# Performance work log

Measured on AMD Instinct MI355X. Metric: run time of the kernel, lower is better.

The kernel has to match this reference:

```python
import jax, jax.numpy as jnp
import numpy as np

NUM_CLASSES = 3
STRIDES = (8, 16, 32)


def _decode(out, stride):
    # out: [B, 5+C, H, W] -> [B, H*W, 5+C] decoded to image coords; also return grid [H*W, 2]
    B, C, H, W = out.shape
    yv, xv = jnp.meshgrid(jnp.arange(H), jnp.arange(W), indexing='ij')
    grid = jnp.stack([xv, yv], -1).reshape(H * W, 2).astype(out.dtype)
    o = out.reshape(B, C, H * W).transpose(0, 2, 1)
    xy = (o[..., :2] + grid[None]) * stride
    wh = jnp.exp(o[..., 2:4]) * stride
    return jnp.concatenate([xy, wh, o[..., 4:]], -1), grid


def _pairwise_iou(gt, pr):
    # gt [G,4], pr [A,4], cxcywh -> iou [G,A]
    tl = jnp.maximum(gt[:, None, :2] - gt[:, None, 2:] / 2, pr[None, :, :2] - pr[None, :, 2:] / 2)
    br = jnp.minimum(gt[:, None, :2] + gt[:, None, 2:] / 2, pr[None, :, :2] + pr[None, :, 2:] / 2)
    en = (tl < br).all(-1).astype(gt.dtype)
    area_i = jnp.prod(br - tl, -1) * en
    area_u = jnp.prod(gt[:, None, 2:], -1) + jnp.prod(pr[None, :, 2:], -1) - area_i
    return area_i / (area_u + 1e-16)


def _iou_loss(pred, target):
    # elementwise IOUloss (loss_type='iou'): 1 - iou^2, shapes [..., 4]
    tl = jnp.maximum(pred[..., :2] - pred[..., 2:] / 2, target[..., :2] - target[..., 2:] / 2)
    br = jnp.minimum(pred[..., :2] + pred[..., 2:] / 2, target[..., :2] + target[..., 2:] / 2)
    en = (tl < br).all(-1).astype(pred.dtype)
    area_i = jnp.prod(br - tl, -1) * en
    area_u = jnp.prod(pred[..., 2:], -1) + jnp.prod(target[..., 2:], -1) - area_i
    iou = area_i / (area_u + 1e-16)
    return 1.0 - iou ** 2


def _bce_logits(x, y):
    # stable BCEWithLogits, reduction='none'
    return jnp.maximum(x, 0) - x * y + jnp.log1p(jnp.exp(-jnp.abs(x)))


def _assign(gt_boxes, gt_cls, box_p, cls_p, obj_p, xs, ys, strides):
    # SimOTA for one image. gt_boxes [G,4], gt_cls [G], box_p [A,4], cls_p [A,C], obj_p [A,1]
    G = gt_boxes.shape[0]
    C = cls_p.shape[-1]
    xc = (xs + 0.5) * strides  # [A] anchor centers in image coords
    yc = (ys + 0.5) * strides
    # anchors inside gt boxes
    gl = gt_boxes[:, 0:1] - gt_boxes[:, 2:3] / 2
    gr = gt_boxes[:, 0:1] + gt_boxes[:, 2:3] / 2
    gt_ = gt_boxes[:, 1:2] - gt_boxes[:, 3:4] / 2
    gb = gt_boxes[:, 1:2] + gt_boxes[:, 3:4] / 2
    in_box = (xc[None] > gl) & (xc[None] < gr) & (yc[None] > gt_) & (yc[None] < gb)  # [G,A]
    # anchors inside center radius 2.5 * stride
    r = 2.5
    in_ctr = ((xc[None] > gt_boxes[:, 0:1] - r * strides[None]) &
              (xc[None] < gt_boxes[:, 0:1] + r * strides[None]) &
              (yc[None] > gt_boxes[:, 1:2] - r * strides[None]) &
              (yc[None] < gt_boxes[:, 1:2] + r * strides[None]))
    cand = in_box.any(0) | in_ctr.any(0)  # [A] candidate anchors (fg_mask)
    in_both = in_box & in_ctr  # [G,A]
    ious = jnp.where(cand[None], _pairwise_iou(gt_boxes, box_p), 0.0)
    iou_cost = -jnp.log(ious + 1e-8)
    p = jnp.sqrt(jax.nn.sigmoid(cls_p) * jax.nn.sigmoid(obj_p))  # [A,C]
    y = jax.nn.one_hot(gt_cls, C, dtype=p.dtype)  # [G,C]
    cls_cost = -(jnp.einsum('gc,ac->ga', y, jnp.log(p + 1e-8)) +
                 jnp.einsum('gc,ac->ga', 1 - y, jnp.log(1 - p + 1e-8)))
    cost = cls_cost + 3.0 * iou_cost + 1e5 * (~in_both).astype(p.dtype)
    cost = jnp.where(cand[None], cost, 1e9)
    # dynamic-k: k_g = clamp(int(sum of top-10 ious), 1)
    topk_ious, _ = jax.lax.top_k(ious, 10)
    dyn_k = jnp.clip(topk_ious.sum(-1).astype(jnp.int32), 1, None)  # [G]
    ranks = jnp.argsort(jnp.argsort(cost, axis=1), axis=1)
    matching = (ranks < dyn_k[:, None]) & cand[None]  # [G,A]
    # resolve anchors matched to multiple gts by min cost
    multi = matching.sum(0) > 1  # [A]
    best = jnp.arange(G)[:, None] == jnp.argmin(cost, axis=0)[None]  # [G,A]
    matching = jnp.where(multi[None], best, matching)
    fg = matching.any(0)  # [A]
    matched_gt = jnp.argmax(matching, axis=0)  # [A]
    pred_iou = (matching.astype(p.dtype) * ious).sum(0)  # [A]
    cls_t = jax.nn.one_hot(gt_cls[matched_gt], C, dtype=p.dtype) * pred_iou[:, None]  # [A,C]
    reg_t = gt_boxes[matched_gt]  # [A,4]
    return fg, cls_t, reg_t


def _forward(p3, p4, p5, mask_inputs, labels, input_images, mask_labels, now_epoch):
    outs, grids, str_list = [], [], []
    for o, s in zip((p3, p4, p5), STRIDES):
        dec, g = _decode(o, float(s))
        outs.append(dec)
        grids.append(g)
        str_list.append(jnp.full((g.shape[0],), float(s), dtype=dec.dtype))
    outputs = jnp.concatenate(outs, 1)  # [B, A, 5+C]
    xs = jnp.concatenate([g[:, 0] for g in grids], 0)  # [A]
    ys = jnp.concatenate([g[:, 1] for g in grids], 0)
    strides = jnp.concatenate(str_list, 0)
    box_p = outputs[..., :4]
    obj_p = outputs[..., 4:5]
    cls_p = outputs[..., 5:]
    gt_boxes = labels[..., :4]
    gt_cls = labels[..., 4].astype(jnp.int32)
    fg, cls_t, reg_t = jax.vmap(_assign, in_axes=(0, 0, 0, 0, 0, None, None, None))(
        gt_boxes, gt_cls, box_p, cls_p, obj_p, xs, ys, strides)
    # assignment is @torch.no_grad() in the original
    fg, cls_t, reg_t = jax.lax.stop_gradient((fg, cls_t, reg_t))
    fgf = fg.astype(outputs.dtype)  # [B,A]
    num_fg = jnp.maximum(fgf.sum(), 1.0)
    loss_iou = (_iou_loss(box_p, reg_t) * fgf).sum()
    loss_obj = _bce_logits(obj_p[..., 0], fgf).sum()
    loss_cls = (_bce_logits(cls_p, cls_t) * fgf[..., None]).sum()
    # segmentation losses: CE (mean NLL over pixels) + Dice
    logp = jax.nn.log_softmax(mask_inputs, axis=1)  # [B,C,H,W]
    ce = -jnp.take_along_axis(logp, mask_labels[:, None].astype(jnp.int32), axis=1).mean()
    sm = jax.nn.softmax(mask_inputs, axis=1).transpose(0, 2, 3, 1)  # [B,H,W,C]
    oh = jax.nn.one_hot(mask_labels, NUM_CLASSES + 1, dtype=sm.dtype)[..., :NUM_CLASSES]
    tp = (oh * sm).sum((0, 1, 2))
    fp = sm.sum((0, 1, 2)) - tp
    fn = oh.sum((0, 1, 2)) - tp
    smooth = 1e-5
    dice = 1.0 - jnp.mean((2 * tp + smooth) / (2 * tp + fn + fp + smooth))  # beta=1
    loss_mask = ce + dice
    loss_sc = jnp.zeros((), outputs.dtype)  # is_sc=False
    reg_w = 5.0
    total = (reg_w * loss_iou + loss_obj + loss_cls + loss_sc) / num_fg + loss_mask
    return jnp.stack([total, reg_w * loss_iou / num_fg, loss_obj / num_fg,
                      loss_cls / num_fg, loss_mask, loss_sc / num_fg])


def setup_inputs() -> dict:
    key = jax.random.key(0)
    ks = jax.random.split(key, 8)
    B, IMG, G = 8, 1024, 20
    C5 = NUM_CLASSES + 5
    p3 = jax.random.normal(ks[0], (B, C5, 128, 128), jnp.float32)
    p4 = jax.random.normal(ks[1], (B, C5, 64, 64), jnp.float32)
    p5 = jax.random.normal(ks[2], (B, C5, 32, 32), jnp.float32)
    mask_inputs = jax.random.normal(ks[3], (B, NUM_CLASSES, IMG, IMG), jnp.float32)
    cxy = jax.random.uniform(ks[4], (B, G, 2), jnp.float32, 64.0, float(IMG - 64))
    wh = jax.random.uniform(ks[5], (B, G, 2), jnp.float32, 16.0, 256.0)
    cls = jax.random.randint(ks[6], (B, G, 1), 0, NUM_CLASSES).astype(jnp.float32)
    labels = jnp.concatenate([cxy, wh, cls], -1)  # [B,G,5] (cx,cy,w,h,class)
    input_images = jax.random.uniform(ks[7], (B, 1, IMG, IMG), jnp.float32)
    mask_labels = jax.random.randint(jax.random.fold_in(key, 9), (B, IMG, IMG), 0, NUM_CLASSES)
    return {"p3": p3, "p4": p4, "p5": p5, "mask_inputs": mask_inputs,
            "labels": labels, "input_images": input_images,
            "mask_labels": mask_labels, "now_epoch": 0}


def reference(p3, p4, p5, mask_inputs, labels, input_images, mask_labels, now_epoch):
    return _forward(p3, p4, p5, mask_inputs, labels, input_images, mask_labels, now_epoch)
```

## Files before the change

### kernel.cpp

```cpp
#include <hip/hip_runtime.h>
#include <cfloat>

constexpr int A_TOT = 21504;
constexpr int NB    = 8;
constexpr int NG    = 20;
constexpr int HW_M  = 1 << 20;
constexpr int SPLIT = 16;
constexpr int CHUNK = A_TOT / SPLIT;
constexpr int MBLK  = 2048;
constexpr int MSLC  = MBLK / 4;

constexpr float L2E = 1.44269504088896340736f;
constexpr float LN2 = 0.69314718055994530942f;

constexpr size_t OFF_DEC  = 0;
constexpr size_t SZ_DEC   = (size_t)NB * A_TOT * 8;
constexpr size_t OFF_IOUS = OFF_DEC + SZ_DEC;
constexpr size_t SZ_GA    = (size_t)NB * NG * A_TOT;
constexpr size_t OFF_COST = OFF_IOUS + SZ_GA;
constexpr size_t OFF_THRC = OFF_COST + SZ_GA;
constexpr size_t OFF_THRI = OFF_THRC + NB * NG;
constexpr size_t OFF_CAND = OFF_THRI + NB * NG;
constexpr size_t OFF_PM   = OFF_CAND + (NB * A_TOT) / 4;
constexpr size_t OFF_PK   = OFF_PM + 672 * 4;
constexpr size_t OFF_PV   = OFF_PK + (size_t)MBLK * 10;
constexpr size_t SZ_PART  = (size_t)NB * NG * SPLIT * 10;
constexpr size_t OFF_PC   = OFF_PV + SZ_PART;
constexpr size_t OFF_PI   = OFF_PC + SZ_PART;

__device__ __forceinline__ float hw_exp2(float x) { return __builtin_amdgcn_exp2f(x); }
__device__ __forceinline__ float hw_log2(float x) { return __builtin_amdgcn_logf(x); }
__device__ __forceinline__ float fexp(float x) { return hw_exp2(x * L2E); }
__device__ __forceinline__ float flog(float x) { return hw_log2(x) * LN2; }
__device__ __forceinline__ float frcp(float x) { return __builtin_amdgcn_rcpf(x); }
__device__ __forceinline__ float fsig(float x) { return frcp(1.f + fexp(-x)); }
__device__ __forceinline__ float fbce(float x, float y) {
  float t = hw_exp2(-fabsf(x) * L2E);
  return fmaxf(x, 0.f) - x * y + LN2 * hw_log2(1.f + t);
}
__device__ __forceinline__ void anchor_geom(int a, int& hw, int& lw, float& st) {
  if (a < 16384)      { hw = a;         lw = 7; st = 8.f;  }
  else if (a < 20480) { hw = a - 16384; lw = 6; st = 16.f; }
  else                { hw = a - 20480; lw = 5; st = 32.f; }
}

__device__ __forceinline__ void merge_desc(float* a, const float* b) {
  float m[16];
  m[0] = a[0]; m[1] = a[1]; m[2] = a[2]; m[3] = a[3]; m[4] = a[4]; m[5] = a[5];
  m[6] = fmaxf(a[6], b[9]); m[7] = fmaxf(a[7], b[8]);
  m[8] = fmaxf(a[8], b[7]); m[9] = fmaxf(a[9], b[6]);
  m[10] = b[5]; m[11] = b[4]; m[12] = b[3]; m[13] = b[2]; m[14] = b[1]; m[15] = b[0];
#pragma unroll
  for (int s = 8; s >= 1; s >>= 1) {
#pragma unroll
    for (int i = 0; i < 16; ++i) {
      if (!(i & s)) {
        float hi = fmaxf(m[i], m[i + s]);
        float lo = fminf(m[i], m[i + s]);
        m[i] = hi; m[i + s] = lo;
      }
    }
  }
#pragma unroll
  for (int j = 0; j < 10; ++j) a[j] = m[j];
}

__device__ __forceinline__ void merge_asc(float* ac, int* ai,
                                          const float* bc, const int* bi) {
  float mc[16]; int mi[16];
#pragma unroll
  for (int i = 0; i < 6; ++i) { mc[i] = ac[i]; mi[i] = ai[i]; }
#pragma unroll
  for (int i = 6; i < 10; ++i) {
    float c2 = bc[15 - i]; int i2 = bi[15 - i];
    bool ta = (ac[i] < c2) || (ac[i] == c2 && ai[i] < i2);
    mc[i] = ta ? ac[i] : c2; mi[i] = ta ? ai[i] : i2;
  }
  mc[10] = bc[5]; mi[10] = bi[5]; mc[11] = bc[4]; mi[11] = bi[4];
  mc[12] = bc[3]; mi[12] = bi[3]; mc[13] = bc[2]; mi[13] = bi[2];
  mc[14] = bc[1]; mi[14] = bi[1]; mc[15] = bc[0]; mi[15] = bi[0];
#pragma unroll
  for (int s = 8; s >= 1; s >>= 1) {
#pragma unroll
    for (int i = 0; i < 16; ++i) {
      if (!(i & s)) {
        float cA = mc[i], cB = mc[i + s];
        int   iA = mi[i], iB = mi[i + s];
        bool ta = (cB < cA) || (cB == cA && iB < iA);
        mc[i]     = ta ? cB : cA; mi[i]     = ta ? iB : iA;
        mc[i + s] = ta ? cA : cB; mi[i + s] = ta ? iA : iB;
      }
    }
  }
#pragma unroll
  for (int j = 0; j < 10; ++j) { ac[j] = mc[j]; ai[j] = mi[j]; }
}

__device__ __forceinline__ void mask_block(int vblk,
    const float* __restrict__ mi, const int* __restrict__ ml,
    float* __restrict__ pk, int tid) {
  int b  = vblk >> 8;
  int g0 = (vblk & 255) << 10;
  const float* base0 = mi + (size_t)b * 3 * HW_M + (size_t)g0 * 4;
  const int*   lbase = ml + ((size_t)b << 20) + (size_t)g0 * 4;

  float4 x0[4], x1[4], x2[4]; int4 lb[4];
#pragma unroll
  for (int u = 0; u < 4; ++u) {
    size_t off = (size_t)(tid + u * 256) * 4;
    x0[u] = *(const float4*)(base0 + off);
    x1[u] = *(const float4*)(base0 + HW_M + off);
    x2[u] = *(const float4*)(base0 + 2 * HW_M + off);
    lb[u] = *(const int4*)(lbase + off);
  }

  float ce = 0.f, tp0 = 0, tp1 = 0, tp2 = 0;
  float ss0 = 0, ss1 = 0, c0 = 0, c1 = 0;

  auto proc = [&](float v0, float v1, float v2, int l) {
    float e0 = hw_exp2(v0 * L2E);
    float e1 = hw_exp2(v1 * L2E);
    float e2 = hw_exp2(v2 * L2E);
    float sum = e0 + e1 + e2;
    float inv = __builtin_amdgcn_rcpf(sum);
    float lse = hw_log2(sum) * LN2;
    float s0 = e0 * inv, s1 = e1 * inv;
    ss0 += s0; ss1 += s1;
    bool l0 = (l == 0), l1 = (l == 1);
    float vl = l0 ? v0 : (l1 ? v1 : v2);
    float el = l0 ? e0 : (l1 ? e1 : e2);
    float sl = el * inv;
    ce += vl - lse;
    tp0 += l0 ? sl : 0.f;
    tp1 += l1 ? sl : 0.f;
    tp2 += (!l0 && !l1) ? sl : 0.f;
    c0 += l0 ? 1.f : 0.f;
    c1 += l1 ? 1.f : 0.f;
  };

#pragma unroll
  for (int u = 0; u < 4; ++u) {
    proc(x0[u].x, x1[u].x, x2[u].x, lb[u].x);
    proc(x0[u].y, x1[u].y, x2[u].y, lb[u].y);
    proc(x0[u].z, x1[u].z, x2[u].z, lb[u].z);
    proc(x0[u].w, x1[u].w, x2[u].w, lb[u].w);
  }
  float ss2 = 16.f - ss0 - ss1;
  float c2 = 16.f - c0 - c1;

  __shared__ float scr[4][10];
  float vals[10] = { ce, tp0, tp1, tp2, ss0, ss1, ss2, c0, c1, c2 };
#pragma unroll
  for (int k = 0; k < 10; ++k) {
    float v = vals[k];
#pragma unroll
    for (int off = 32; off > 0; off >>= 1) v += __shfl_down(v, off, 64);
    if ((tid & 63) == 0) scr[tid >> 6][k] = v;
  }
  __syncthreads();
  if (tid == 0) {
#pragma unroll
    for (int k = 0; k < 10; ++k)
      pk[(size_t)vblk * 10 + k] = scr[0][k] + scr[1][k] + scr[2][k] + scr[3][k];
  }
}

__global__ __launch_bounds__(256) void k_cost_mask(
    const float* __restrict__ p3, const float* __restrict__ p4,
    const float* __restrict__ p5, const float* __restrict__ labels,
    float* __restrict__ dec, float* __restrict__ ious,
    float* __restrict__ cost, unsigned char* __restrict__ cand,
    const float* __restrict__ mi, const int* __restrict__ ml,
    float* __restrict__ pk) {
  int bi = blockIdx.x, tid = threadIdx.x;
  if (bi >= 672) { mask_block(bi - 672, mi, ml, pk, tid); return; }
  int b = bi / 84, cx = bi - b * 84;

  __shared__ float gt[NG][5];
  if (tid < NG * 5) ((float*)gt)[tid] = labels[b * NG * 5 + tid];
  __syncthreads();
  int a = cx * 256 + tid;

  int hw, lw; float st;
  anchor_geom(a, hw, lw, st);
  const float* src; int HW;
  if (a < 16384)      { src = p3; HW = 16384; }
  else if (a < 20480) { src = p4; HW = 4096;  }
  else                { src = p5; HW = 1024;  }
  int x = hw & ((1 << lw) - 1), y = hw >> lw;
  const float* c0 = src + (size_t)b * 8 * HW + hw;
  float o0 = c0[0];
  float o1 = c0[(size_t)HW];
  float o2 = c0[(size_t)2 * HW];
  float o3 = c0[(size_t)3 * HW];
  float o4 = c0[(size_t)4 * HW];
  float o5 = c0[(size_t)5 * HW];
  float o6 = c0[(size_t)6 * HW];
  float o7 = c0[(size_t)7 * HW];
  float px = (o0 + (float)x) * st, py = (o1 + (float)y) * st;
  float pw = fexp(o2) * st,        ph = fexp(o3) * st;
  {
    float4* dst = (float4*)(dec + ((size_t)b * A_TOT + a) * 8);
    dst[0] = make_float4(px, py, pw, ph);
    dst[1] = make_float4(o4, o5, o6, o7);
  }

  float xc = ((float)x + 0.5f) * st, yc = ((float)y + 0.5f) * st;

  float so = fsig(o4);
  float cc0, cc1, cc2, S;
  {
    float q0 = sqrtf(fsig(o5) * so);
    float q1 = sqrtf(fsig(o6) * so);
    float q2 = sqrtf(fsig(o7) * so);
    float lg0 = flog(q0 + 1e-8f), lg1 = flog(q1 + 1e-8f), lg2 = flog(q2 + 1e-8f);
    float m0 = flog(1.f - q0 + 1e-8f), m1 = flog(1.f - q1 + 1e-8f), m2 = flog(1.f - q2 + 1e-8f);
    S = m0 + m1 + m2;
    cc0 = lg0 - m0; cc1 = lg1 - m1; cc2 = lg2 - m2;
  }

  float iouv[NG];
  unsigned bothMask = 0;
  bool anyBox = false, anyCtr = false;
  float hpw = pw * 0.5f, hph = ph * 0.5f;
  float plx = px - hpw, prx = px + hpw, pty = py - hph, pby = py + hph;
  float parea = pw * ph;
  float r = 2.5f * st;

#pragma unroll
  for (int g = 0; g < NG; ++g) {
    float gx = gt[g][0], gy = gt[g][1], gw = gt[g][2], gh = gt[g][3];
    float hgw = gw * 0.5f, hgh = gh * 0.5f;
    float glx = gx - hgw, grx = gx + hgw, gty = gy - hgh, gby = gy + hgh;
    bool ib = (xc > glx) && (xc < grx) && (yc > gty) && (yc < gby);
    bool ic = (xc > gx - r) && (xc < gx + r) && (yc > gy - r) && (yc < gy + r);
    anyBox |= ib; anyCtr |= ic;
    if (ib && ic) bothMask |= (1u << g);
    float tlx = fmaxf(glx, plx), brx = fminf(grx, prx);
    float tly = fmaxf(gty, pty), bry = fminf(gby, pby);
    float en = ((tlx < brx) && (tly < bry)) ? 1.f : 0.f;
    float ai = (brx - tlx) * (bry - tly) * en;
    float au = gw * gh + parea - ai;
    iouv[g] = ai / (au + 1e-16f);
  }
  bool cd = anyBox || anyCtr;
  cand[(size_t)b * A_TOT + a] = cd ? 1 : 0;

#pragma unroll
  for (int g = 0; g < NG; ++g) {
    float iv = cd ? iouv[g] : 0.f;
    int cg = (int)gt[g][4];
    float ccg = (cg == 0) ? cc0 : ((cg == 1) ? cc1 : cc2);
    float c = -(ccg + S) - 3.f * flog(iv + 1e-8f) +
              (((bothMask >> g) & 1u) ? 0.f : 100000.f);
    size_t idx = ((size_t)(b * NG + g)) * A_TOT + a;
    ious[idx] = iv;
    cost[idx] = cd ? c : 1e9f;
  }
}

__global__ __launch_bounds__(256) void k_topk_mask(
    const float* __restrict__ ious, const float* __restrict__ cost,
    float* __restrict__ pV, float* __restrict__ pC, int* __restrict__ pI,
    const float* __restrict__ mi, const int* __restrict__ ml,
    float* __restrict__ pk) {
  int bi = blockIdx.x, tid = threadIdx.x;
  if (bi >= 640) { mask_block(MSLC + (bi - 640), mi, ml, pk, tid); return; }

  int w = tid >> 6, lane = tid & 63;
  int t = bi * 4 + w;
  int b = t / (NG * SPLIT);
  int rem = t - b * (NG * SPLIT);
  int g = rem / SPLIT;
  int s = rem - g * SPLIT;
  int row = b * NG + g;
  int lo = s * CHUNK;
  const float4* iou4 = (const float4*)(ious + (size_t)row * A_TOT + lo);
  const float4* cst4 = (const float4*)(cost + (size_t)row * A_TOT + lo);
  constexpr int NG4 = CHUNK / 4;

  float tv[10];
  float tc[10]; int ti[10];
#pragma unroll
  for (int j = 0; j < 10; ++j) { tv[j] = -1e30f; tc[j] = FLT_MAX; ti[j] = 0x7fffffff; }

  auto insV = [&](float v) {
    if (v > tv[9]) {
#pragma unroll
      for (int j = 0; j < 10; ++j)
        if (v > tv[j]) { float t2 = tv[j]; tv[j] = v; v = t2; }
    }
  };
  auto insC = [&](float c, int ii) {
    if ((c < tc[9]) || (c == tc[9] && ii < ti[9])) {
#pragma unroll
      for (int j = 0; j < 10; ++j) {
        bool lt = (c < tc[j]) || (c == tc[j] && ii < ti[j]);
        if (lt) {
          float t2 = tc[j]; tc[j] = c; c = t2;
          int t3 = ti[j]; ti[j] = ii; ii = t3;
        }
      }
    }
  };

#pragma unroll 1
  for (int grp = lane; grp < NG4; grp += 64) {
    float4 v4 = iou4[grp];
    float4 c4 = cst4[grp];
    int base = lo + grp * 4;
    insV(v4.x); insV(v4.y); insV(v4.z); insV(v4.w);
    insC(c4.x, base); insC(c4.y, base + 1); insC(c4.z, base + 2); insC(c4.w, base + 3);
  }

#pragma unroll 1
  for (int d = 1; d < 64; d <<= 1) {
    float bv[10];
#pragma unroll
    for (int j = 0; j < 10; ++j) bv[j] = __shfl_xor(tv[j], d, 64);
    merge_desc(tv, bv);
  }
#pragma unroll 1
  for (int d = 1; d < 64; d <<= 1) {
    float bc[10]; int bi2[10];
#pragma unroll
    for (int j = 0; j < 10; ++j) {
      bc[j] = __shfl_xor(tc[j], d, 64);
      bi2[j] = __shfl_xor(ti[j], d, 64);
    }
    merge_asc(tc, ti, bc, bi2);
  }

  if (lane == 0) {
    size_t base = ((size_t)row * SPLIT + s) * 10;
#pragma unroll
    for (int j = 0; j < 10; ++j) {
      pV[base + j] = tv[j];
      pC[base + j] = tc[j];
      pI[base + j] = ti[j];
    }
  }
}

__global__ __launch_bounds__(256) void k_merge_mask(
    const float* __restrict__ pV, const float* __restrict__ pC,
    const int* __restrict__ pI, float* __restrict__ thrC, int* __restrict__ thrI,
    const float* __restrict__ mi, const int* __restrict__ ml,
    float* __restrict__ pk) {
  int bi = blockIdx.x, tid = threadIdx.x;
  if (bi >= 160) { mask_block(2 * MSLC + (bi - 160), mi, ml, pk, tid); return; }
  int row = bi;
  constexpr int NC = SPLIT * 10;
  __shared__ float sV[NC], sC[NC];
  __shared__ int   sI[NC];
  __shared__ float slot[10];
  __shared__ int kS;

  if (tid < NC) {
    size_t base = (size_t)row * NC + tid;
    sV[tid] = pV[base];
    sC[tid] = pC[base];
    sI[tid] = pI[base];
  }
  __syncthreads();

  float myV = 0.f, myC = 0.f; int myI = 0, rankV = 0;
  if (tid < NC) {
    myV = sV[tid]; myC = sC[tid]; myI = sI[tid];
    for (int j = 0; j < NC; ++j) {
      float v = sV[j];
      rankV += ((v > myV) || (v == myV && j < tid)) ? 1 : 0;
    }
  }
  if (tid < NC && rankV < 10) slot[rankV] = myV;
  __syncthreads();
  if (tid == 0) {
    float sum = 0.f;
#pragma unroll
    for (int j = 0; j < 10; ++j) sum += slot[j];
    int k = (int)sum; if (k < 1) k = 1;
    kS = k;
  }
  __syncthreads();
  if (tid < NC) {
    int rankC = 0;
    for (int j = 0; j < NC; ++j) {
      float c = sC[j];
      rankC += ((c < myC) || (c == myC && sI[j] < myI)) ? 1 : 0;
    }
    if (rankC == kS - 1) { thrC[row] = myC; thrI[row] = myI; }
  }
}

__global__ __launch_bounds__(256) void k_match_mask(
    const float* __restrict__ dec, const float* __restrict__ labels,
    const float* __restrict__ ious, const float* __restrict__ cost,
    const unsigned char* __restrict__ cand,
    const float* __restrict__ thrC, const int* __restrict__ thrI,
    float* __restrict__ pm,
    const float* __restrict__ mi, const int* __restrict__ ml,
    float* __restrict__ pk) {
  int bi = blockIdx.x, tid = threadIdx.x;
  if (bi >= 672) { mask_block(3 * MSLC + (bi - 672), mi, ml, pk, tid); return; }
  int b = bi / 84, cx = bi - b * 84;

  __shared__ float gt[NG][5];
  __shared__ float tC[NG];
  __shared__ int   tI[NG];
  if (tid < NG * 5) ((float*)gt)[tid] = labels[b * NG * 5 + tid];
  if (tid >= 128 && tid < 128 + NG) tC[tid - 128] = thrC[b * NG + tid - 128];
  if (tid >= 160 && tid < 160 + NG) tI[tid - 160] = thrI[b * NG + tid - 160];
  __syncthreads();
  int a = cx * 256 + tid;

  bool cd = cand[(size_t)b * A_TOT + a] != 0;
  int cnt = 0, firstg = -1, gmin = 0;
  float minc = FLT_MAX, pisum = 0.f, iou_gmin = 0.f;
#pragma unroll
  for (int g = 0; g < NG; ++g) {
    size_t idx = ((size_t)(b * NG + g)) * A_TOT + a;
    float c = cost[idx];
    float iv = ious[idx];
    if (c < minc) { minc = c; gmin = g; iou_gmin = iv; }
    bool m = cd && ((c < tC[g]) || (c == tC[g] && a <= tI[g]));
    if (m) { cnt++; if (firstg < 0) firstg = g; pisum += iv; }
  }
  if (cnt > 1) { firstg = gmin; pisum = iou_gmin; }
  bool fg = cnt > 0;

  const float4* dp = (const float4*)(dec + ((size_t)b * A_TOT + a) * 8);
  float4 d0 = dp[0], d1 = dp[1];
  float l_obj = fbce(d1.x, fg ? 1.f : 0.f);
  float l_iou = 0.f, l_cls = 0.f, nfg = fg ? 1.f : 0.f;
  if (fg) {
    float gx = gt[firstg][0], gy = gt[firstg][1];
    float gw = gt[firstg][2], gh = gt[firstg][3];
    int cg = (int)gt[firstg][4];
    float px = d0.x, py = d0.y, pw = d0.z, ph = d0.w;
    float tlx = fmaxf(px - pw * 0.5f, gx - gw * 0.5f);
    float brx = fminf(px + pw * 0.5f, gx + gw * 0.5f);
    float tly = fmaxf(py - ph * 0.5f, gy - gh * 0.5f);
    float bry = fminf(py + ph * 0.5f, gy + gh * 0.5f);
    float en = ((tlx < brx) && (tly < bry)) ? 1.f : 0.f;
    float ai = (brx - tlx) * (bry - tly) * en;
    float au = pw * ph + gw * gh - ai;
    float iou = ai / (au + 1e-16f);
    l_iou = 1.f - iou * iou;
    l_cls  = fbce(d1.y, (cg == 0) ? pisum : 0.f);
    l_cls += fbce(d1.z, (cg == 1) ? pisum : 0.f);
    l_cls += fbce(d1.w, (cg == 2) ? pisum : 0.f);
  }

  __shared__ float scr2[4][4];
  float vals[4] = { nfg, l_iou, l_obj, l_cls };
#pragma unroll
  for (int k = 0; k < 4; ++k) {
    float v = vals[k];
#pragma unroll
    for (int off = 32; off > 0; off >>= 1) v += __shfl_down(v, off, 64);
    if ((tid & 63) == 0) scr2[tid >> 6][k] = v;
  }
  __syncthreads();
  if (tid == 0) {
#pragma unroll
    for (int k = 0; k < 4; ++k)
      pm[(size_t)bi * 4 + k] = scr2[0][k] + scr2[1][k] + scr2[2][k] + scr2[3][k];
  }
}

__device__ __forceinline__ float bsum256(float v, float* scr) {
#pragma unroll
  for (int off = 32; off > 0; off >>= 1) v += __shfl_down(v, off, 64);
  __syncthreads();
  if ((threadIdx.x & 63) == 0) scr[threadIdx.x >> 6] = v;
  __syncthreads();
  return scr[0] + scr[1] + scr[2] + scr[3];
}

__global__ __launch_bounds__(256) void k_final(
    const float* __restrict__ pm, const float* __restrict__ pk,
    float* __restrict__ out) {
  __shared__ float scr[4];
  int tid = threadIdx.x;
  float t0 = 0, t1 = 0, t2 = 0, t3 = 0;
  for (int r = tid; r < 672; r += 256) {
    t0 += pm[(size_t)r * 4 + 0];
    t1 += pm[(size_t)r * 4 + 1];
    t2 += pm[(size_t)r * 4 + 2];
    t3 += pm[(size_t)r * 4 + 3];
  }
  float u[10] = {0,0,0,0,0,0,0,0,0,0};
  for (int r = tid; r < MBLK; r += 256) {
#pragma unroll
    for (int k = 0; k < 10; ++k) u[k] += pk[(size_t)r * 10 + k];
  }
  float S_nfg = bsum256(t0, scr);
  float S_iou = bsum256(t1, scr);
  float S_obj = bsum256(t2, scr);
  float S_cls = bsum256(t3, scr);
  float S_ce  = bsum256(u[0], scr);
  float S_tp0 = bsum256(u[1], scr);
  float S_tp1 = bsum256(u[2], scr);
  float S_tp2 = bsum256(u[3], scr);
  float S_ss0 = bsum256(u[4], scr);
  float S_ss1 = bsum256(u[5], scr);
  float S_ss2 = bsum256(u[6], scr);
  float S_c0  = bsum256(u[7], scr);
  float S_c1  = bsum256(u[8], scr);
  float S_c2  = bsum256(u[9], scr);

  if (tid == 0) {
    float nfg = fmaxf(S_nfg, 1.f);
    float o1 = 5.f * S_iou / nfg;
    float o2 = S_obj / nfg;
    float o3 = S_cls / nfg;
    float ce = -S_ce / (float)((long long)NB << 20);
    float tps[3] = { S_tp0, S_tp1, S_tp2 };
    float sss[3] = { S_ss0, S_ss1, S_ss2 };
    float cns[3] = { S_c0, S_c1, S_c2 };
    float ds = 0.f;
#pragma unroll
    for (int c = 0; c < 3; ++c) {
      float tp = tps[c];
      float fp = sss[c] - tp;
      float fn = cns[c] - tp;
      ds += (2.f * tp + 1e-5f) / (2.f * tp + fn + fp + 1e-5f);
    }
    float dice = 1.f - ds / 3.f;
    float o4 = ce + dice;
    out[0] = o1 + o2 + o3 + o4;
    out[1] = o1;
    out[2] = o2;
    out[3] = o3;
    out[4] = o4;
    out[5] = 0.f;
  }
}

extern "C" void kernel_launch(void* const* d_in, const int* in_sizes, int n_in,
                              void* d_out, int out_size, void* d_ws, size_t ws_size,
                              hipStream_t stream) {
  const float* p3     = (const float*)d_in[0];
  const float* p4     = (const float*)d_in[1];
  const float* p5     = (const float*)d_in[2];
  const float* mi     = (const float*)d_in[3];
  const float* labels = (const float*)d_in[4];
  const int*   ml     = (const int*)d_in[6];

  float* ws   = (float*)d_ws;
  float* dec  = ws + OFF_DEC;
  float* ious = ws + OFF_IOUS;
  float* cost = ws + OFF_COST;
  float* thrC = ws + OFF_THRC;
  int*   thrI = (int*)(ws + OFF_THRI);
  unsigned char* cand = (unsigned char*)(ws + OFF_CAND);
  float* pm   = ws + OFF_PM;
  float* pk   = ws + OFF_PK;
  float* pV   = ws + OFF_PV;
  float* pC   = ws + OFF_PC;
  int*   pI   = (int*)(ws + OFF_PI);
  float* out  = (float*)d_out;

  k_cost_mask <<<672 + MSLC, 256, 0, stream>>>(p3, p4, p5, labels, dec, ious,
                                               cost, cand, mi, ml, pk);
  k_topk_mask <<<640 + MSLC, 256, 0, stream>>>(ious, cost, pV, pC, pI,
                                               mi, ml, pk);
  k_merge_mask<<<160 + MSLC, 256, 0, stream>>>(pV, pC, pI, thrC, thrI,
                                               mi, ml, pk);
  k_match_mask<<<672 + MSLC, 256, 0, stream>>>(dec, labels, ious, cost, cand,
                                               thrC, thrI, pm, mi, ml, pk);
  k_final<<<1, 256, 0, stream>>>(pm, pk, out);
}
```

Before: 91.40 us.

## Fuse top-k split and merge into one kernel, recompute decode in match

Merges the per-chunk top-k and the merge kernels into a single kernel in which one block per (image, gt) row scans the whole anchor row and merges the four wave results in shared memory. This removes a launch and the partial-result round trip. The match kernel now reloads the raw predictions and recomputes the decode, candidate mask and IoUs instead of reading the dec, cand and ious buffers, so those workspace writes and reads are dropped. The mask-loss block split across the three kernels is rebalanced to 680/688/680. The cost is that 160 blocks now each do a long serial scan, and the match kernel repeats the IoU computation.

Result: slower. 123.1 us (+34.7%).

```diff
diff --git a/kernel.cpp b/kernel.cpp
--- a/kernel.cpp
+++ b/kernel.cpp
@@ -5,28 +5,22 @@
 constexpr int NB    = 8;
 constexpr int NG    = 20;
 constexpr int HW_M  = 1 << 20;
-constexpr int SPLIT = 16;
-constexpr int CHUNK = A_TOT / SPLIT;
+constexpr int NGRP4 = A_TOT / 4;
 constexpr int MBLK  = 2048;
-constexpr int MSLC  = MBLK / 4;
+constexpr int MS1   = 680;
+constexpr int MS2   = 688;
+constexpr int MS3   = 680;
 
 constexpr float L2E = 1.44269504088896340736f;
 constexpr float LN2 = 0.69314718055994530942f;
 
-constexpr size_t OFF_DEC  = 0;
-constexpr size_t SZ_DEC   = (size_t)NB * A_TOT * 8;
-constexpr size_t OFF_IOUS = OFF_DEC + SZ_DEC;
 constexpr size_t SZ_GA    = (size_t)NB * NG * A_TOT;
+constexpr size_t OFF_IOUS = 0;
 constexpr size_t OFF_COST = OFF_IOUS + SZ_GA;
 constexpr size_t OFF_THRC = OFF_COST + SZ_GA;
 constexpr size_t OFF_THRI = OFF_THRC + NB * NG;
-constexpr size_t OFF_CAND = OFF_THRI + NB * NG;
-constexpr size_t OFF_PM   = OFF_CAND + (NB * A_TOT) / 4;
+constexpr size_t OFF_PM   = OFF_THRI + NB * NG;
 constexpr size_t OFF_PK   = OFF_PM + 672 * 4;
-constexpr size_t OFF_PV   = OFF_PK + (size_t)MBLK * 10;
-constexpr size_t SZ_PART  = (size_t)NB * NG * SPLIT * 10;
-constexpr size_t OFF_PC   = OFF_PV + SZ_PART;
-constexpr size_t OFF_PI   = OFF_PC + SZ_PART;
 
 __device__ __forceinline__ float hw_exp2(float x) { return __builtin_amdgcn_exp2f(x); }
 __device__ __forceinline__ float hw_log2(float x) { return __builtin_amdgcn_logf(x); }
@@ -95,6 +89,7 @@
 #pragma unroll
   for (int j = 0; j < 10; ++j) { ac[j] = mc[j]; ai[j] = mi[j]; }
 }
+
 
 __device__ __forceinline__ void mask_block(int vblk,
     const float* __restrict__ mi, const int* __restrict__ ml,
@@ -168,8 +163,7 @@
 __global__ __launch_bounds__(256) void k_cost_mask(
     const float* __restrict__ p3, const float* __restrict__ p4,
     const float* __restrict__ p5, const float* __restrict__ labels,
-    float* __restrict__ dec, float* __restrict__ ious,
-    float* __restrict__ cost, unsigned char* __restrict__ cand,
+    float* __restrict__ ious, float* __restrict__ cost,
     const float* __restrict__ mi, const int* __restrict__ ml,
     float* __restrict__ pk) {
   int bi = blockIdx.x, tid = threadIdx.x;
@@ -199,11 +193,6 @@
   float o7 = c0[(size_t)7 * HW];
   float px = (o0 + (float)x) * st, py = (o1 + (float)y) * st;
   float pw = fexp(o2) * st,        ph = fexp(o3) * st;
-  {
-    float4* dst = (float4*)(dec + ((size_t)b * A_TOT + a) * 8);
-    dst[0] = make_float4(px, py, pw, ph);
-    dst[1] = make_float4(o4, o5, o6, o7);
-  }
 
   float xc = ((float)x + 0.5f) * st, yc = ((float)y + 0.5f) * st;
 
@@ -244,7 +233,6 @@
     iouv[g] = ai / (au + 1e-16f);
   }
   bool cd = anyBox || anyCtr;
-  cand[(size_t)b * A_TOT + a] = cd ? 1 : 0;
 
 #pragma unroll
   for (int g = 0; g < NG; ++g) {
@@ -259,25 +247,16 @@
   }
 }
 
-__global__ __launch_bounds__(256) void k_topk_mask(
+__global__ __launch_bounds__(256) void k_topkmerge_mask(
     const float* __restrict__ ious, const float* __restrict__ cost,
-    float* __restrict__ pV, float* __restrict__ pC, int* __restrict__ pI,
+    float* __restrict__ thrC, int* __restrict__ thrI,
     const float* __restrict__ mi, const int* __restrict__ ml,
     float* __restrict__ pk) {
   int bi = blockIdx.x, tid = threadIdx.x;
-  if (bi >= 640) { mask_block(MSLC + (bi - 640), mi, ml, pk, tid); return; }
-
-  int w = tid >> 6, lane = tid & 63;
-  int t = bi * 4 + w;
-  int b = t / (NG * SPLIT);
-  int rem = t - b * (NG * SPLIT);
-  int g = rem / SPLIT;
-  int s = rem - g * SPLIT;
-  int row = b * NG + g;
-  int lo = s * CHUNK;
-  const float4* iou4 = (const float4*)(ious + (size_t)row * A_TOT + lo);
-  const float4* cst4 = (const float4*)(cost + (size_t)row * A_TOT + lo);
-  constexpr int NG4 = CHUNK / 4;
+  if (bi >= 160) { mask_block(MS1 + (bi - 160), mi, ml, pk, tid); return; }
+  int row = bi;
+  const float4* iou4 = (const float4*)(ious + (size_t)row * A_TOT);
+  const float4* cst4 = (const float4*)(cost + (size_t)row * A_TOT);
 
   float tv[10];
   float tc[10]; int ti[10];
@@ -305,10 +284,10 @@
   };
 
 #pragma unroll 1
-  for (int grp = lane; grp < NG4; grp += 64) {
+  for (int grp = tid; grp < NGRP4; grp += 256) {
     float4 v4 = iou4[grp];
     float4 c4 = cst4[grp];
-    int base = lo + grp * 4;
+    int base = grp * 4;
     insV(v4.x); insV(v4.y); insV(v4.z); insV(v4.w);
     insC(c4.x, base); insC(c4.y, base + 1); insC(c4.z, base + 2); insC(c4.w, base + 3);
   }
@@ -331,48 +310,29 @@
     merge_asc(tc, ti, bc, bi2);
   }
 
-  if (lane == 0) {
-    size_t base = ((size_t)row * SPLIT + s) * 10;
-#pragma unroll
-    for (int j = 0; j < 10; ++j) {
-      pV[base + j] = tv[j];
-      pC[base + j] = tc[j];
-      pI[base + j] = ti[j];
-    }
-  }
-}
-
-__global__ __launch_bounds__(256) void k_merge_mask(
-    const float* __restrict__ pV, const float* __restrict__ pC,
-    const int* __restrict__ pI, float* __restrict__ thrC, int* __restrict__ thrI,
-    const float* __restrict__ mi, const int* __restrict__ ml,
-    float* __restrict__ pk) {
-  int bi = blockIdx.x, tid = threadIdx.x;
-  if (bi >= 160) { mask_block(2 * MSLC + (bi - 160), mi, ml, pk, tid); return; }
-  int row = bi;
-  constexpr int NC = SPLIT * 10;
-  __shared__ float sV[NC], sC[NC];
-  __shared__ int   sI[NC];
+  __shared__ float sV[40], sC[40];
+  __shared__ int   sI[40];
   __shared__ float slot[10];
   __shared__ int kS;
-
-  if (tid < NC) {
-    size_t base = (size_t)row * NC + tid;
-    sV[tid] = pV[base];
-    sC[tid] = pC[base];
-    sI[tid] = pI[base];
-  }
-  __syncthreads();
-
-  float myV = 0.f, myC = 0.f; int myI = 0, rankV = 0;
-  if (tid < NC) {
-    myV = sV[tid]; myC = sC[tid]; myI = sI[tid];
-    for (int j = 0; j < NC; ++j) {
+  int w = tid >> 6;
+  if ((tid & 63) == 0) {
+#pragma unroll
+    for (int j = 0; j < 10; ++j) {
+      sV[w * 10 + j] = tv[j];
+      sC[w * 10 + j] = tc[j];
+      sI[w * 10 + j] = ti[j];
+    }
+  }
+  __syncthreads();
+  if (tid < 40) {
+    float myV = sV[tid];
+    int rankV = 0;
+    for (int j = 0; j < 40; ++j) {
       float v = sV[j];
       rankV += ((v > myV) || (v == myV && j < tid)) ? 1 : 0;
     }
-  }
-  if (tid < NC && rankV < 10) slot[rankV] = myV;
+    if (rankV < 10) slot[rankV] = myV;
+  }
   __syncthreads();
   if (tid == 0) {
     float sum = 0.f;
@@ -382,9 +342,10 @@
     kS = k;
   }
   __syncthreads();
-  if (tid < NC) {
+  if (tid < 40) {
+    float myC = sC[tid]; int myI = sI[tid];
     int rankC = 0;
-    for (int j = 0; j < NC; ++j) {
+    for (int j = 0; j < 40; ++j) {
       float c = sC[j];
       rankC += ((c < myC) || (c == myC && sI[j] < myI)) ? 1 : 0;
     }
@@ -393,15 +354,15 @@
 }
 
 __global__ __launch_bounds__(256) void k_match_mask(
-    const float* __restrict__ dec, const float* __restrict__ labels,
-    const float* __restrict__ ious, const float* __restrict__ cost,
-    const unsigned char* __restrict__ cand,
+    const float* __restrict__ p3, const float* __restrict__ p4,
+    const float* __restrict__ p5, const float* __restrict__ labels,
+    const float* __restrict__ cost,
     const float* __restrict__ thrC, const int* __restrict__ thrI,
     float* __restrict__ pm,
     const float* __restrict__ mi, const int* __restrict__ ml,
     float* __restrict__ pk) {
   int bi = blockIdx.x, tid = threadIdx.x;
-  if (bi >= 672) { mask_block(3 * MSLC + (bi - 672), mi, ml, pk, tid); return; }
+  if (bi >= 672) { mask_block(MS1 + MS2 + (bi - 672), mi, ml, pk, tid); return; }
   int b = bi / 84, cx = bi - b * 84;
 
   __shared__ float gt[NG][5];
@@ -413,14 +374,57 @@
   __syncthreads();
   int a = cx * 256 + tid;
 
-  bool cd = cand[(size_t)b * A_TOT + a] != 0;
+  int hw, lw; float st;
+  anchor_geom(a, hw, lw, st);
+  const float* src; int HW;
+  if (a < 16384)      { src = p3; HW = 16384; }
+  else if (a < 20480) { src = p4; HW = 4096;  }
+  else                { src = p5; HW = 1024;  }
+  int x = hw & ((1 << lw) - 1), y = hw >> lw;
+  const float* c0p = src + (size_t)b * 8 * HW + hw;
+  float o0 = c0p[0];
+  float o1 = c0p[(size_t)HW];
+  float o2 = c0p[(size_t)2 * HW];
+  float o3 = c0p[(size_t)3 * HW];
+  float o4 = c0p[(size_t)4 * HW];
+  float o5 = c0p[(size_t)5 * HW];
+  float o6 = c0p[(size_t)6 * HW];
+  float o7 = c0p[(size_t)7 * HW];
+  float px = (o0 + (float)x) * st, py = (o1 + (float)y) * st;
+  float pw = fexp(o2) * st,        ph = fexp(o3) * st;
+
+  float xc = ((float)x + 0.5f) * st, yc = ((float)y + 0.5f) * st;
+
+  float iouv[NG];
+  bool anyBox = false, anyCtr = false;
+  float hpw = pw * 0.5f, hph = ph * 0.5f;
+  float plx = px - hpw, prx = px + hpw, pty = py - hph, pby = py + hph;
+  float parea = pw * ph;
+  float r = 2.5f * st;
+#pragma unroll
+  for (int g = 0; g < NG; ++g) {
+    float gx = gt[g][0], gy = gt[g][1], gw = gt[g][2], gh = gt[g][3];
+    float hgw = gw * 0.5f, hgh = gh * 0.5f;
+    float glx = gx - hgw, grx = gx + hgw, gty = gy - hgh, gby = gy + hgh;
+    bool ib = (xc > glx) && (xc < grx) && (yc > gty) && (yc < gby);
+    bool ic = (xc > gx - r) && (xc < gx + r) && (yc > gy - r) && (yc < gy + r);
+    anyBox |= ib; anyCtr |= ic;
+    float tlx = fmaxf(glx, plx), brx = fminf(grx, prx);
+    float tly = fmaxf(gty, pty), bry = fminf(gby, pby);
+    float en = ((tlx < brx) && (tly < bry)) ? 1.f : 0.f;
+    float ai = (brx - tlx) * (bry - tly) * en;
+    float au = gw * gh + parea - ai;
+    iouv[g] = ai / (au + 1e-16f);
+  }
+  bool cd = anyBox || anyCtr;
+
   int cnt = 0, firstg = -1, gmin = 0;
   float minc = FLT_MAX, pisum = 0.f, iou_gmin = 0.f;
 #pragma unroll
   for (int g = 0; g < NG; ++g) {
     size_t idx = ((size_t)(b * NG + g)) * A_TOT + a;
     float c = cost[idx];
-    float iv = ious[idx];
+    float iv = cd ? iouv[g] : 0.f;
     if (c < minc) { minc = c; gmin = g; iou_gmin = iv; }
     bool m = cd && ((c < tC[g]) || (c == tC[g] && a <= tI[g]));
     if (m) { cnt++; if (firstg < 0) firstg = g; pisum += iv; }
@@ -428,15 +432,12 @@
   if (cnt > 1) { firstg = gmin; pisum = iou_gmin; }
   bool fg = cnt > 0;
 
-  const float4* dp = (const float4*)(dec + ((size_t)b * A_TOT + a) * 8);
-  float4 d0 = dp[0], d1 = dp[1];
-  float l_obj = fbce(d1.x, fg ? 1.f : 0.f);
+  float l_obj = fbce(o4, fg ? 1.f : 0.f);
   float l_iou = 0.f, l_cls = 0.f, nfg = fg ? 1.f : 0.f;
   if (fg) {
     float gx = gt[firstg][0], gy = gt[firstg][1];
     float gw = gt[firstg][2], gh = gt[firstg][3];
     int cg = (int)gt[firstg][4];
-    float px = d0.x, py = d0.y, pw = d0.z, ph = d0.w;
     float tlx = fmaxf(px - pw * 0.5f, gx - gw * 0.5f);
     float brx = fminf(px + pw * 0.5f, gx + gw * 0.5f);
     float tly = fmaxf(py - ph * 0.5f, gy - gh * 0.5f);
@@ -446,9 +447,9 @@
     float au = pw * ph + gw * gh - ai;
     float iou = ai / (au + 1e-16f);
     l_iou = 1.f - iou * iou;
-    l_cls  = fbce(d1.y, (cg == 0) ? pisum : 0.f);
-    l_cls += fbce(d1.z, (cg == 1) ? pisum : 0.f);
-    l_cls += fbce(d1.w, (cg == 2) ? pisum : 0.f);
+    l_cls  = fbce(o5, (cg == 0) ? pisum : 0.f);
+    l_cls += fbce(o6, (cg == 1) ? pisum : 0.f);
+    l_cls += fbce(o7, (cg == 2) ? pisum : 0.f);
   }
 
   __shared__ float scr2[4][4];
@@ -548,26 +549,19 @@
   const int*   ml     = (const int*)d_in[6];
 
   float* ws   = (float*)d_ws;
-  float* dec  = ws + OFF_DEC;
   float* ious = ws + OFF_IOUS;
   float* cost = ws + OFF_COST;
   float* thrC = ws + OFF_THRC;
   int*   thrI = (int*)(ws + OFF_THRI);
-  unsigned char* cand = (unsigned char*)(ws + OFF_CAND);
   float* pm   = ws + OFF_PM;
   float* pk   = ws + OFF_PK;
-  float* pV   = ws + OFF_PV;
-  float* pC   = ws + OFF_PC;
-  int*   pI   = (int*)(ws + OFF_PI);
   float* out  = (float*)d_out;
 
-  k_cost_mask <<<672 + MSLC, 256, 0, stream>>>(p3, p4, p5, labels, dec, ious,
-                                               cost, cand, mi, ml, pk);
-  k_topk_mask <<<640 + MSLC, 256, 0, stream>>>(ious, cost, pV, pC, pI,
-                                               mi, ml, pk);
-  k_merge_mask<<<160 + MSLC, 256, 0, stream>>>(pV, pC, pI, thrC, thrI,
-                                               mi, ml, pk);
-  k_match_mask<<<672 + MSLC, 256, 0, stream>>>(dec, labels, ious, cost, cand,
-                                               thrC, thrI, pm, mi, ml, pk);
+  k_cost_mask     <<<672 + MS1, 256, 0, stream>>>(p3, p4, p5, labels, ious,
+                                                  cost, mi, ml, pk);
+  k_topkmerge_mask<<<160 + MS2, 256, 0, stream>>>(ious, cost, thrC, thrI,
+                                                  mi, ml, pk);
+  k_match_mask    <<<672 + MS3, 256, 0, stream>>>(p3, p4, p5, labels, cost,
+                                                  thrC, thrI, pm, mi, ml, pk);
   k_final<<<1, 256, 0, stream>>>(pm, pk, out);
 }
```

## Fuse top-k and merge kernels into one 1024-thread block per row

Applied to the files above, without the earlier changes.

Merges the per-chunk top-k kernel and the merge kernel into a single kernel in which one 1024-thread block handles a whole (image, gt) row, with its 16 waves each scanning one chunk and exchanging partial top-10 lists through shared memory instead of global buffers. This removes one kernel launch and the global partial-result round trip. The mask-loss work that was spread over four launches is redistributed across the remaining three, with the middle kernel packing four mask sub-blocks per 1024-thread block. Larger blocks may lower occupancy and scheduling flexibility, and the top-k phase now runs on only 160 blocks.

Result: slower. 96.96 us (+6.1%).

```diff
diff --git a/kernel.cpp b/kernel.cpp
--- a/kernel.cpp
+++ b/kernel.cpp
@@ -8,7 +8,8 @@
 constexpr int SPLIT = 16;
 constexpr int CHUNK = A_TOT / SPLIT;
 constexpr int MBLK  = 2048;
-constexpr int MSLC  = MBLK / 4;
+constexpr int MS1 = 684, MS2 = 680, MS4 = 684;
+constexpr int MOFF1 = 0, MOFF2 = 684, MOFF4 = 1364;
 
 constexpr float L2E = 1.44269504088896340736f;
 constexpr float LN2 = 0.69314718055994530942f;
@@ -23,10 +24,6 @@
 constexpr size_t OFF_CAND = OFF_THRI + NB * NG;
 constexpr size_t OFF_PM   = OFF_CAND + (NB * A_TOT) / 4;
 constexpr size_t OFF_PK   = OFF_PM + 672 * 4;
-constexpr size_t OFF_PV   = OFF_PK + (size_t)MBLK * 10;
-constexpr size_t SZ_PART  = (size_t)NB * NG * SPLIT * 10;
-constexpr size_t OFF_PC   = OFF_PV + SZ_PART;
-constexpr size_t OFF_PI   = OFF_PC + SZ_PART;
 
 __device__ __forceinline__ float hw_exp2(float x) { return __builtin_amdgcn_exp2f(x); }
 __device__ __forceinline__ float hw_log2(float x) { return __builtin_amdgcn_logf(x); }
@@ -96,9 +93,9 @@
   for (int j = 0; j < 10; ++j) { ac[j] = mc[j]; ai[j] = mi[j]; }
 }
 
-__device__ __forceinline__ void mask_block(int vblk,
+__device__ __forceinline__ void mask_core(int vblk,
     const float* __restrict__ mi, const int* __restrict__ ml,
-    float* __restrict__ pk, int tid) {
+    float* __restrict__ pk, int tid256, float (*scr)[10], int gw) {
   int b  = vblk >> 8;
   int g0 = (vblk & 255) << 10;
   const float* base0 = mi + (size_t)b * 3 * HW_M + (size_t)g0 * 4;
@@ -107,7 +104,7 @@
   float4 x0[4], x1[4], x2[4]; int4 lb[4];
 #pragma unroll
   for (int u = 0; u < 4; ++u) {
-    size_t off = (size_t)(tid + u * 256) * 4;
+    size_t off = (size_t)(tid256 + u * 256) * 4;
     x0[u] = *(const float4*)(base0 + off);
     x1[u] = *(const float4*)(base0 + HW_M + off);
     x2[u] = *(const float4*)(base0 + 2 * HW_M + off);
@@ -148,21 +145,28 @@
   float ss2 = 16.f - ss0 - ss1;
   float c2 = 16.f - c0 - c1;
 
-  __shared__ float scr[4][10];
   float vals[10] = { ce, tp0, tp1, tp2, ss0, ss1, ss2, c0, c1, c2 };
 #pragma unroll
   for (int k = 0; k < 10; ++k) {
     float v = vals[k];
 #pragma unroll
     for (int off = 32; off > 0; off >>= 1) v += __shfl_down(v, off, 64);
-    if ((tid & 63) == 0) scr[tid >> 6][k] = v;
-  }
-  __syncthreads();
-  if (tid == 0) {
+    if ((tid256 & 63) == 0) scr[gw + (tid256 >> 6)][k] = v;
+  }
+  __syncthreads();
+  if (tid256 == 0) {
 #pragma unroll
     for (int k = 0; k < 10; ++k)
-      pk[(size_t)vblk * 10 + k] = scr[0][k] + scr[1][k] + scr[2][k] + scr[3][k];
-  }
+      pk[(size_t)vblk * 10 + k] = scr[gw][k] + scr[gw + 1][k] +
+                                  scr[gw + 2][k] + scr[gw + 3][k];
+  }
+}
+
+__device__ __forceinline__ void mask_block(int vblk,
+    const float* __restrict__ mi, const int* __restrict__ ml,
+    float* __restrict__ pk, int tid) {
+  __shared__ float scr[4][10];
+  mask_core(vblk, mi, ml, pk, tid, scr, 0);
 }
 
 __global__ __launch_bounds__(256) void k_cost_mask(
@@ -173,7 +177,7 @@
     const float* __restrict__ mi, const int* __restrict__ ml,
     float* __restrict__ pk) {
   int bi = blockIdx.x, tid = threadIdx.x;
-  if (bi >= 672) { mask_block(bi - 672, mi, ml, pk, tid); return; }
+  if (bi >= 672) { mask_block(MOFF1 + (bi - 672), mi, ml, pk, tid); return; }
   int b = bi / 84, cx = bi - b * 84;
 
   __shared__ float gt[NG][5];
@@ -259,21 +263,21 @@
   }
 }
 
-__global__ __launch_bounds__(256) void k_topk_mask(
+__global__ __launch_bounds__(1024) void k_topkmerge_mask(
     const float* __restrict__ ious, const float* __restrict__ cost,
-    float* __restrict__ pV, float* __restrict__ pC, int* __restrict__ pI,
+    float* __restrict__ thrC, int* __restrict__ thrI,
     const float* __restrict__ mi, const int* __restrict__ ml,
     float* __restrict__ pk) {
   int bi = blockIdx.x, tid = threadIdx.x;
-  if (bi >= 640) { mask_block(MSLC + (bi - 640), mi, ml, pk, tid); return; }
-
+  if (bi >= 160) {
+    __shared__ float mscr[16][10];
+    int vblk = MOFF2 + (bi - 160) * 4 + (tid >> 8);
+    mask_core(vblk, mi, ml, pk, tid & 255, mscr, (tid >> 8) * 4);
+    return;
+  }
+  int row = bi;
   int w = tid >> 6, lane = tid & 63;
-  int t = bi * 4 + w;
-  int b = t / (NG * SPLIT);
-  int rem = t - b * (NG * SPLIT);
-  int g = rem / SPLIT;
-  int s = rem - g * SPLIT;
-  int row = b * NG + g;
+  int s = w;
   int lo = s * CHUNK;
   const float4* iou4 = (const float4*)(ious + (size_t)row * A_TOT + lo);
   const float4* cst4 = (const float4*)(cost + (size_t)row * A_TOT + lo);
@@ -331,36 +335,18 @@
     merge_asc(tc, ti, bc, bi2);
   }
 
-  if (lane == 0) {
-    size_t base = ((size_t)row * SPLIT + s) * 10;
-#pragma unroll
-    for (int j = 0; j < 10; ++j) {
-      pV[base + j] = tv[j];
-      pC[base + j] = tc[j];
-      pI[base + j] = ti[j];
-    }
-  }
-}
-
-__global__ __launch_bounds__(256) void k_merge_mask(
-    const float* __restrict__ pV, const float* __restrict__ pC,
-    const int* __restrict__ pI, float* __restrict__ thrC, int* __restrict__ thrI,
-    const float* __restrict__ mi, const int* __restrict__ ml,
-    float* __restrict__ pk) {
-  int bi = blockIdx.x, tid = threadIdx.x;
-  if (bi >= 160) { mask_block(2 * MSLC + (bi - 160), mi, ml, pk, tid); return; }
-  int row = bi;
   constexpr int NC = SPLIT * 10;
   __shared__ float sV[NC], sC[NC];
   __shared__ int   sI[NC];
   __shared__ float slot[10];
   __shared__ int kS;
-
-  if (tid < NC) {
-    size_t base = (size_t)row * NC + tid;
-    sV[tid] = pV[base];
-    sC[tid] = pC[base];
-    sI[tid] = pI[base];
+  if (lane == 0) {
+#pragma unroll
+    for (int j = 0; j < 10; ++j) {
+      sV[s * 10 + j] = tv[j];
+      sC[s * 10 + j] = tc[j];
+      sI[s * 10 + j] = ti[j];
+    }
   }
   __syncthreads();
 
@@ -401,7 +387,7 @@
     const float* __restrict__ mi, const int* __restrict__ ml,
     float* __restrict__ pk) {
   int bi = blockIdx.x, tid = threadIdx.x;
-  if (bi >= 672) { mask_block(3 * MSLC + (bi - 672), mi, ml, pk, tid); return; }
+  if (bi >= 672) { mask_block(MOFF4 + (bi - 672), mi, ml, pk, tid); return; }
   int b = bi / 84, cx = bi - b * 84;
 
   __shared__ float gt[NG][5];
@@ -556,18 +542,13 @@
   unsigned char* cand = (unsigned char*)(ws + OFF_CAND);
   float* pm   = ws + OFF_PM;
   float* pk   = ws + OFF_PK;
-  float* pV   = ws + OFF_PV;
-  float* pC   = ws + OFF_PC;
-  int*   pI   = (int*)(ws + OFF_PI);
   float* out  = (float*)d_out;
 
-  k_cost_mask <<<672 + MSLC, 256, 0, stream>>>(p3, p4, p5, labels, dec, ious,
-                                               cost, cand, mi, ml, pk);
-  k_topk_mask <<<640 + MSLC, 256, 0, stream>>>(ious, cost, pV, pC, pI,
-                                               mi, ml, pk);
-  k_merge_mask<<<160 + MSLC, 256, 0, stream>>>(pV, pC, pI, thrC, thrI,
-                                               mi, ml, pk);
-  k_match_mask<<<672 + MSLC, 256, 0, stream>>>(dec, labels, ious, cost, cand,
-                                               thrC, thrI, pm, mi, ml, pk);
+  k_cost_mask     <<<672 + MS1, 256, 0, stream>>>(p3, p4, p5, labels, dec, ious,
+                                                  cost, cand, mi, ml, pk);
+  k_topkmerge_mask<<<160 + MS2 / 4, 1024, 0, stream>>>(ious, cost, thrC, thrI,
+                                                       mi, ml, pk);
+  k_match_mask    <<<672 + MS4, 256, 0, stream>>>(dec, labels, ious, cost, cand,
+                                                  thrC, thrI, pm, mi, ml, pk);
   k_final<<<1, 256, 0, stream>>>(pm, pk, out);
 }
```
